# Kernel tuning notes

Measured on AMD Instinct MI355X. Metric: run time of the kernel, lower is better.

## Reference

```python
import jax, jax.numpy as jnp
import numpy as np

N, M, D = 8192, 32768, 256

def setup_inputs() -> dict:
    key = jax.random.key(0)
    k1, k2 = jax.random.split(key)
    image_embs = jax.random.normal(k1, (N, D), dtype=jnp.float32)
    text_embs = jax.random.normal(k2, (M, D), dtype=jnp.float32)
    return {"image_embs": image_embs, "text_embs": text_embs, "k": 10}

def reference(image_embs, text_embs, k):
    # sims: [N, M] similarity matrix (cosine if inputs are pre-normalized)
    sims = image_embs @ text_embs.T
    _, idx = jax.lax.top_k(sims, k)
    return idx.astype(jnp.int32)
```

## Files before the change

kernel.cpp:

```cpp
#include <hip/hip_runtime.h>
#include <hip/hip_bf16.h>
#include <stdint.h>

#define N_ROWS 8192
#define M_COLS 32768
#define D_DIM  256
#define KSEL   10
#define THRMUL 2.75f
#define SEG    40
#define NSEGS  8
#define CSLOT  5
#define NKEEP  16
#define NPAD   32

typedef __bf16              bf16x8 __attribute__((ext_vector_type(8)));
typedef float               f32x4  __attribute__((ext_vector_type(4)));
typedef unsigned short      u16x8  __attribute__((ext_vector_type(8)));
typedef unsigned long long  u64;

__device__ __forceinline__ unsigned short f2bf_rne(float f) {
  unsigned u = __float_as_uint(f);
  u += 0x7FFFu + ((u >> 16) & 1u);
  return (unsigned short)(u >> 16);
}

__device__ __forceinline__ int lanecount_lt(unsigned long long m) {
  return __builtin_amdgcn_mbcnt_hi((unsigned)(m >> 32),
                                   __builtin_amdgcn_mbcnt_lo((unsigned)m, 0));
}

#if __has_builtin(__builtin_amdgcn_global_load_lds)
typedef const __attribute__((address_space(1))) char* gp_t;
typedef __attribute__((address_space(3)))       char* lp_t;
#endif

__device__ __forceinline__ void stage64k(const char* __restrict__ gsrc,
                                         unsigned short* lds, int wid, int lane) {
#if __has_builtin(__builtin_amdgcn_global_load_lds)
#pragma unroll
  for (int i = 0; i < 16; ++i) {
    int off = (wid * 16 + i) * 1024 + lane * 16;
    __builtin_amdgcn_global_load_lds((gp_t)(gsrc + off), (lp_t)((char*)lds + off),
                                     16, 0, 0);
  }
#else
  const u16x8* __restrict__ s = (const u16x8*)gsrc;
  u16x8* d = (u16x8*)lds;
  int t = wid * 64 + lane;
#pragma unroll
  for (int i = 0; i < 16; ++i) d[t + i * 256] = s[t + i * 256];
#endif
}

__global__ __launch_bounds__(256, 2) void cvt_swz_kernel(
    const float* __restrict__ inA, unsigned short* __restrict__ outA,
    const float* __restrict__ inB, unsigned short* __restrict__ outB,
    float* __restrict__ thr) {
  __shared__ alignas(16) unsigned short sm[4224 * 8];
  const int tid = threadIdx.x;
  const int isA = blockIdx.x < (N_ROWS / 128);
  const int tile = isA ? blockIdx.x : blockIdx.x - (N_ROWS / 128);
  const float4* __restrict__ src =
      (const float4*)((isA ? inA : inB) + (size_t)tile * 128 * D_DIM);
  u16x8* __restrict__ dst =
      (u16x8*)((isA ? outA : outB) + (size_t)tile * 128 * D_DIM);

#pragma unroll
  for (int i = 0; i < 16; ++i) {
    int u = i * 256 + tid;
    float4 a = src[u * 2], b = src[u * 2 + 1];
    u16x8 o;
    o[0] = f2bf_rne(a.x); o[1] = f2bf_rne(a.y); o[2] = f2bf_rne(a.z); o[3] = f2bf_rne(a.w);
    o[4] = f2bf_rne(b.x); o[5] = f2bf_rne(b.y); o[6] = f2bf_rne(b.z); o[7] = f2bf_rne(b.w);
    ((u16x8*)sm)[u + (u >> 5)] = o;
  }
  __syncthreads();
#pragma unroll
  for (int i = 0; i < 16; ++i) {
    int o = i * 256 + tid;
    int g = o >> 9, s = (o >> 6) & 7, q = (o >> 4) & 3, m = o & 15;
    int u = ((g * 16 + m) << 5) + s * 4 + q;
    dst[o] = ((const u16x8*)sm)[u + (u >> 5)];
  }

  if (isA) {
    int row = tid >> 1, half = tid & 1;
    const float4* __restrict__ rp =
        (const float4*)(inA + ((size_t)tile * 128 + row) * D_DIM + half * 128);
    float s = 0.f;
#pragma unroll
    for (int j = 0; j < 32; ++j) {
      float4 a = rp[j];
      s += a.x * a.x + a.y * a.y + a.z * a.z + a.w * a.w;
    }
    s += __shfl_xor(s, 1);
    if (half == 0) thr[tile * 128 + row] = THRMUL * sqrtf(s);
  }
}

__global__ __launch_bounds__(256, 2) void gemm_filter_kernel(
    const unsigned short* __restrict__ Ab, const unsigned short* __restrict__ Bb,
    const float* __restrict__ thr,
    int* __restrict__ cnt_seg, u64* __restrict__ cand) {
  __shared__ alignas(16) unsigned short sm[32 * 1024];
  __shared__ float    thr_s[128];
  __shared__ unsigned lcnt[128];

  const int tid  = threadIdx.x;
  const int lane = tid & 63;
  const int wid  = tid >> 6;
  const int wm   = wid >> 1;
  const int wn   = wid & 1;
  const int quad = lane >> 4;
  const int m16  = lane & 15;

  const int bid    = blockIdx.x;
  const int msplit = bid & 7;
  const int rowb   = bid >> 3;
  const int row0   = rowb * 128;
  const int rot    = (bid * 23) & 63;

  stage64k((const char*)Ab + (size_t)rowb * 65536, sm, wid, lane);
  if (tid < 128) { thr_s[tid] = thr[row0 + tid]; lcnt[tid] = 0u; }
  __syncthreads();

  bf16x8 afrag[4][8];
#pragma unroll
  for (int tm = 0; tm < 4; ++tm)
#pragma unroll
    for (int s = 0; s < 8; ++s)
      afrag[tm][s] = ((const bf16x8*)sm)[(wm * 4 + tm) * 512 + s * 64 + lane];
  float thrv[4][4];
#pragma unroll
  for (int tm = 0; tm < 4; ++tm)
#pragma unroll
    for (int r = 0; r < 4; ++r)
      thrv[tm][r] = thr_s[wm * 64 + tm * 16 + quad * 4 + r];
  __syncthreads();

  const u16x8* __restrict__ Bsplit =
      (const u16x8*)((const char*)Bb + (size_t)msplit * 2097152);
  const f32x4 fzero = {0.f, 0.f, 0.f, 0.f};

  bf16x8 bfrag[8][2];
  {
    const u16x8* __restrict__ Bt = Bsplit + (size_t)rot * 2048;
#pragma unroll
    for (int s = 0; s < 4; ++s)
#pragma unroll
      for (int tn = 0; tn < 2; ++tn)
        bfrag[s][tn] = (bf16x8)Bt[(wn * 2 + tn) * 512 + s * 64 + lane];
  }

  for (int i = 0; i < 64; ++i) {
    const int t   = (rot + i) & 63;
    const int tn2 = (rot + i + 1) & 63;
    const u16x8* __restrict__ Bt = Bsplit + (size_t)t * 2048;
    const u16x8* __restrict__ Bn = Bsplit + (size_t)tn2 * 2048;

    f32x4 acc[4][2];
#pragma unroll
    for (int a_ = 0; a_ < 4; ++a_)
#pragma unroll
      for (int b_ = 0; b_ < 2; ++b_) acc[a_][b_] = fzero;

#pragma unroll
    for (int s = 0; s < 8; ++s) {
      const u16x8* __restrict__ src = (s < 4) ? Bt : Bn;
      const int ss = (s + 4) & 7;
#pragma unroll
      for (int tn = 0; tn < 2; ++tn)
        bfrag[ss][tn] = (bf16x8)src[(wn * 2 + tn) * 512 + ss * 64 + lane];
#pragma unroll
      for (int tm = 0; tm < 4; ++tm)
#pragma unroll
        for (int tn = 0; tn < 2; ++tn)
          acc[tm][tn] = __builtin_amdgcn_mfma_f32_16x16x32_bf16(
              afrag[tm][s], bfrag[s][tn], acc[tm][tn], 0, 0, 0);
    }

#pragma unroll
    for (int tm = 0; tm < 4; ++tm) {
#pragma unroll
      for (int tn = 0; tn < 2; ++tn) {
#pragma unroll
        for (int r = 0; r < 4; ++r) {
          float v = acc[tm][tn][r];
          if (v > thrv[tm][r]) {
            int lrow = wm * 64 + tm * 16 + quad * 4 + r;
            unsigned slot = atomicAdd(&lcnt[lrow], 1u);
            if (slot < SEG) {
              int gcol = msplit * 4096 + t * 64 + wn * 32 + tn * 16 + m16;
              u64 pk = ((u64)__float_as_uint(v) << 32) | (unsigned)gcol;
              cand[((size_t)(row0 + lrow) * NSEGS + msplit) * SEG + slot] = pk;
            }
          }
        }
      }
    }
  }
  __syncthreads();

  if (tid < 128) {
    unsigned c = lcnt[tid];
    cnt_seg[(size_t)(row0 + tid) * NSEGS + msplit] = (int)(c < SEG ? c : SEG);
  }
}

__global__ __launch_bounds__(256) void select_rescore_kernel(
    const float* __restrict__ A, const float* __restrict__ B,
    const int* __restrict__ cnt_seg, const u64* __restrict__ cand,
    int* __restrict__ out) {
  __shared__ int    sel_s[4][NPAD];
  __shared__ double ex_s[4][NPAD];

  const int wid  = threadIdx.x >> 6;
  const int lane = threadIdx.x & 63;
  const int r    = blockIdx.x * 4 + wid;

  unsigned key[CSLOT];
  int      id[CSLOT];
#pragma unroll
  for (int j = 0; j < CSLOT; ++j) {
    int p   = lane + j * 64;
    int seg = p / SEG;
    int off = p - seg * SEG;
    int c   = cnt_seg[(size_t)r * NSEGS + seg];
    if (off < c) {
      u64 pk = cand[((size_t)r * NSEGS + seg) * SEG + off];
      key[j] = (unsigned)(pk >> 32);
      id[j]  = (int)(unsigned)(pk & 0xffffffffu);
    } else {
      key[j] = 0u;
      id[j]  = 0x7fffffff;
    }
  }

  unsigned cur = 0;
  for (int b = 30; b >= 8; --b) {
    unsigned candk = cur | (1u << b);
    int c = 0;
#pragma unroll
    for (int j = 0; j < CSLOT; ++j)
      c += __popcll(__ballot(key[j] >= candk));
    if (c >= NKEEP) cur = candk;
  }

  int base = 0;
#pragma unroll
  for (int j = 0; j < CSLOT; ++j) {
    unsigned long long m = __ballot(key[j] >= cur && key[j] != 0u);
    int pos = base + lanecount_lt(m);
    if (key[j] >= cur && key[j] != 0u && pos < NPAD) sel_s[wid][pos] = id[j];
    base += __popcll(m);
  }
  int kcount = base < NPAD ? base : NPAD;
  for (int p = kcount + lane; p < NPAD; p += 64) sel_s[wid][p] = -1;
  __syncthreads();

  const int cand4 = lane >> 2;
  const int half  = lane & 3;
  const float4* __restrict__ A4 = (const float4*)A;
  const float4* __restrict__ B4 = (const float4*)B;
#pragma unroll
  for (int pass = 0; pass < 2; ++pass) {
    int slot = pass * 16 + cand4;
    int idx  = sel_s[wid][slot];
    if (idx >= 0) {
      double acc0 = 0.0, acc1 = 0.0;
#pragma unroll
      for (int j = 0; j < 16; ++j) {
        float4 a4 = A4[(size_t)r * 64 + half * 16 + j];
        float4 b4 = B4[(size_t)idx * 64 + half * 16 + j];
        acc0 += (double)a4.x * b4.x + (double)a4.y * b4.y;
        acc1 += (double)a4.z * b4.z + (double)a4.w * b4.w;
      }
      double tot = acc0 + acc1;
      tot += __shfl_xor(tot, 1);
      tot += __shfl_xor(tot, 2);
      if (half == 0) ex_s[wid][slot] = tot;
    } else if (half == 0) {
      ex_s[wid][slot] = -1.0e300;
    }
  }
  __syncthreads();

  double myex = (lane < NPAD) ? ex_s[wid][lane] : -1.0e300;
  int    myid = (lane < NPAD) ? sel_s[wid][lane] : 0x7fffffff;
  if (myid < 0) { myex = -1.0e300; myid = 0x7fffffff; }
#pragma unroll
  for (int p = 0; p < KSEL; ++p) {
    double be = myex; int bi = myid;
    for (int off = 32; off > 0; off >>= 1) {
      double oe = __shfl_xor(be, off);
      int    oi = __shfl_xor(bi, off);
      if (oe > be || (oe == be && oi < bi)) { be = oe; bi = oi; }
    }
    if (lane == 0) out[(size_t)r * KSEL + p] = bi;
    if (myid == bi) { myex = -1.0e300; myid = 0x7fffffff; }
  }
}

extern "C" void kernel_launch(void* const* d_in, const int* in_sizes, int n_in,
                              void* d_out, int out_size, void* d_ws, size_t ws_size,
                              hipStream_t stream) {
  (void)in_sizes; (void)n_in; (void)out_size; (void)ws_size;
  const float* img = (const float*)d_in[0];
  const float* txt = (const float*)d_in[1];
  int* out = (int*)d_out;

  char* ws = (char*)d_ws;
  unsigned short* Ab = (unsigned short*)ws;
  unsigned short* Bb = (unsigned short*)(ws + ((size_t)4 << 20));
  float* thr     = (float*)(ws + ((size_t)20 << 20));
  int*   cnt_seg = (int*)  (ws + ((size_t)20 << 20) + (64 << 10));
  u64*   cand    = (u64*)  (ws + ((size_t)21 << 20));

  cvt_swz_kernel<<<(N_ROWS + M_COLS) / 128, 256, 0, stream>>>(img, Ab, txt, Bb, thr);

  gemm_filter_kernel<<<512, 256, 0, stream>>>(Ab, Bb, thr, cnt_seg, cand);

  select_rescore_kernel<<<N_ROWS / 4, 256, 0, stream>>>(img, txt, cnt_seg, cand, out);
}
```

Before: 291.7 us.

## Switch filter GEMM from bf16 to fp8 e4m3 and widen the rescore candidate set

Inputs are now quantized to fp8 e4m3 instead of bf16, and the filter GEMM uses fp8 MFMA instructions with A fragments loaded straight from global memory rather than staged through LDS. This halves the bytes moved for the converted matrices and doubles MFMA throughput per instruction. To make up for the larger quantization error, the kept candidates per row go from 16 to 32, and the exact fp64 rescore handles 64 padded slots over four passes. The risks are extra rescore work, and candidates being missed if the fp8 error is larger than the threshold margin or the widened selection allows.

```diff
diff --git a/kernel.cpp b/kernel.cpp
--- a/kernel.cpp
+++ b/kernel.cpp
@@ -10,18 +10,33 @@
 #define SEG    40
 #define NSEGS  8
 #define CSLOT  5
-#define NKEEP  16
-#define NPAD   32
-
-typedef __bf16              bf16x8 __attribute__((ext_vector_type(8)));
+#define NKEEP  32
+#define NPAD   64
+
 typedef float               f32x4  __attribute__((ext_vector_type(4)));
-typedef unsigned short      u16x8  __attribute__((ext_vector_type(8)));
 typedef unsigned long long  u64;
 
-__device__ __forceinline__ unsigned short f2bf_rne(float f) {
+__device__ __forceinline__ unsigned char f2e4m3(float f) {
   unsigned u = __float_as_uint(f);
-  u += 0x7FFFu + ((u >> 16) & 1u);
-  return (unsigned short)(u >> 16);
+  unsigned sgn = (u >> 24) & 0x80u;
+  int E = (int)((u >> 23) & 0xffu) - 127;
+  unsigned m = u & 0x7fffffu;
+  if (E >= -6) {
+    unsigned keep = m >> 20;
+    unsigned rest = m & 0xfffffu;
+    keep += (rest > 0x80000u || (rest == 0x80000u && (keep & 1u))) ? 1u : 0u;
+    unsigned val = ((unsigned)(E + 7) << 3) + keep;
+    if (val > 0x7eu) val = 0x7eu;
+    return (unsigned char)(sgn | val);
+  }
+  if (E < -10) return (unsigned char)sgn;
+  unsigned mant = m | 0x800000u;
+  int shift = 23 - (E + 9);
+  unsigned keep = mant >> shift;
+  unsigned rem  = mant & ((1u << shift) - 1u);
+  unsigned half = 1u << (shift - 1);
+  keep += (rem > half || (rem == half && (keep & 1u))) ? 1u : 0u;
+  return (unsigned char)(sgn | keep);
 }
 
 __device__ __forceinline__ int lanecount_lt(unsigned long long m) {
@@ -29,58 +44,40 @@
                                    __builtin_amdgcn_mbcnt_lo((unsigned)m, 0));
 }
 
-#if __has_builtin(__builtin_amdgcn_global_load_lds)
-typedef const __attribute__((address_space(1))) char* gp_t;
-typedef __attribute__((address_space(3)))       char* lp_t;
-#endif
-
-__device__ __forceinline__ void stage64k(const char* __restrict__ gsrc,
-                                         unsigned short* lds, int wid, int lane) {
-#if __has_builtin(__builtin_amdgcn_global_load_lds)
-#pragma unroll
-  for (int i = 0; i < 16; ++i) {
-    int off = (wid * 16 + i) * 1024 + lane * 16;
-    __builtin_amdgcn_global_load_lds((gp_t)(gsrc + off), (lp_t)((char*)lds + off),
-                                     16, 0, 0);
-  }
-#else
-  const u16x8* __restrict__ s = (const u16x8*)gsrc;
-  u16x8* d = (u16x8*)lds;
-  int t = wid * 64 + lane;
-#pragma unroll
-  for (int i = 0; i < 16; ++i) d[t + i * 256] = s[t + i * 256];
-#endif
-}
-
 __global__ __launch_bounds__(256, 2) void cvt_swz_kernel(
-    const float* __restrict__ inA, unsigned short* __restrict__ outA,
-    const float* __restrict__ inB, unsigned short* __restrict__ outB,
+    const float* __restrict__ inA, unsigned char* __restrict__ outA,
+    const float* __restrict__ inB, unsigned char* __restrict__ outB,
     float* __restrict__ thr) {
-  __shared__ alignas(16) unsigned short sm[4224 * 8];
+  __shared__ alignas(16) char sm[128 * 264];
   const int tid = threadIdx.x;
   const int isA = blockIdx.x < (N_ROWS / 128);
   const int tile = isA ? blockIdx.x : blockIdx.x - (N_ROWS / 128);
   const float4* __restrict__ src =
       (const float4*)((isA ? inA : inB) + (size_t)tile * 128 * D_DIM);
-  u16x8* __restrict__ dst =
-      (u16x8*)((isA ? outA : outB) + (size_t)tile * 128 * D_DIM);
-
-#pragma unroll
-  for (int i = 0; i < 16; ++i) {
+  unsigned char* __restrict__ dst = (isA ? outA : outB) + (size_t)tile * 32768;
+
+#pragma unroll
+  for (int i = 0; i < 32; ++i) {
     int u = i * 256 + tid;
-    float4 a = src[u * 2], b = src[u * 2 + 1];
-    u16x8 o;
-    o[0] = f2bf_rne(a.x); o[1] = f2bf_rne(a.y); o[2] = f2bf_rne(a.z); o[3] = f2bf_rne(a.w);
-    o[4] = f2bf_rne(b.x); o[5] = f2bf_rne(b.y); o[6] = f2bf_rne(b.z); o[7] = f2bf_rne(b.w);
-    ((u16x8*)sm)[u + (u >> 5)] = o;
-  }
-  __syncthreads();
-#pragma unroll
-  for (int i = 0; i < 16; ++i) {
-    int o = i * 256 + tid;
-    int g = o >> 9, s = (o >> 6) & 7, q = (o >> 4) & 3, m = o & 15;
-    int u = ((g * 16 + m) << 5) + s * 4 + q;
-    dst[o] = ((const u16x8*)sm)[u + (u >> 5)];
+    float4 a = src[u];
+    int e = u * 4;
+    int row = e >> 8, k = e & 255;
+    unsigned pk = (unsigned)f2e4m3(a.x) | ((unsigned)f2e4m3(a.y) << 8) |
+                  ((unsigned)f2e4m3(a.z) << 16) | ((unsigned)f2e4m3(a.w) << 24);
+    *(unsigned*)(sm + row * 264 + k) = pk;
+  }
+  __syncthreads();
+#pragma unroll
+  for (int i = 0; i < 8; ++i) {
+    int g = i * 256 + tid;
+    int pn = g >> 10, o = g & 1023;
+    int ln = o & 63, s = (o >> 6) & 7, p = o >> 9;
+    int item = pn * 64 + p * 32 + (ln & 15);
+    int k = s * 32 + (ln >> 4) * 8;
+    u64 lo = *(const u64*)(sm + item * 264 + k);
+    u64 hi = *(const u64*)(sm + (item + 16) * 264 + k);
+    ulong2 v; v.x = lo; v.y = hi;
+    *(ulong2*)(dst + (size_t)g * 16) = v;
   }
 
   if (isA) {
@@ -99,10 +96,9 @@
 }
 
 __global__ __launch_bounds__(256, 2) void gemm_filter_kernel(
-    const unsigned short* __restrict__ Ab, const unsigned short* __restrict__ Bb,
+    const ulong2* __restrict__ Ab, const ulong2* __restrict__ Bb,
     const float* __restrict__ thr,
     int* __restrict__ cnt_seg, u64* __restrict__ cand) {
-  __shared__ alignas(16) unsigned short sm[32 * 1024];
   __shared__ float    thr_s[128];
   __shared__ unsigned lcnt[128];
 
@@ -120,43 +116,43 @@
   const int row0   = rowb * 128;
   const int rot    = (bid * 23) & 63;
 
-  stage64k((const char*)Ab + (size_t)rowb * 65536, sm, wid, lane);
   if (tid < 128) { thr_s[tid] = thr[row0 + tid]; lcnt[tid] = 0u; }
-  __syncthreads();
-
-  bf16x8 afrag[4][8];
-#pragma unroll
-  for (int tm = 0; tm < 4; ++tm)
-#pragma unroll
-    for (int s = 0; s < 8; ++s)
-      afrag[tm][s] = ((const bf16x8*)sm)[(wm * 4 + tm) * 512 + s * 64 + lane];
+
+  const ulong2* __restrict__ Ap = Ab + (size_t)(rowb * 2 + wm) * 1024;
+  long long afrag[4][8];
+#pragma unroll
+  for (int h = 0; h < 2; ++h)
+#pragma unroll
+    for (int s = 0; s < 8; ++s) {
+      ulong2 v = Ap[(h * 8 + s) * 64 + lane];
+      afrag[h * 2 + 0][s] = (long long)v.x;
+      afrag[h * 2 + 1][s] = (long long)v.y;
+    }
+
+  __syncthreads();
   float thrv[4][4];
 #pragma unroll
   for (int tm = 0; tm < 4; ++tm)
 #pragma unroll
     for (int r = 0; r < 4; ++r)
       thrv[tm][r] = thr_s[wm * 64 + tm * 16 + quad * 4 + r];
-  __syncthreads();
-
-  const u16x8* __restrict__ Bsplit =
-      (const u16x8*)((const char*)Bb + (size_t)msplit * 2097152);
+
+  const ulong2* __restrict__ Bsplit = Bb + (size_t)msplit * 65536;
   const f32x4 fzero = {0.f, 0.f, 0.f, 0.f};
 
-  bf16x8 bfrag[8][2];
+  ulong2 bfrag[8];
   {
-    const u16x8* __restrict__ Bt = Bsplit + (size_t)rot * 2048;
+    const ulong2* __restrict__ Bt = Bsplit + (size_t)rot * 1024;
 #pragma unroll
     for (int s = 0; s < 4; ++s)
-#pragma unroll
-      for (int tn = 0; tn < 2; ++tn)
-        bfrag[s][tn] = (bf16x8)Bt[(wn * 2 + tn) * 512 + s * 64 + lane];
+      bfrag[s] = Bt[(wn * 8 + s) * 64 + lane];
   }
 
   for (int i = 0; i < 64; ++i) {
     const int t   = (rot + i) & 63;
     const int tn2 = (rot + i + 1) & 63;
-    const u16x8* __restrict__ Bt = Bsplit + (size_t)t * 2048;
-    const u16x8* __restrict__ Bn = Bsplit + (size_t)tn2 * 2048;
+    const ulong2* __restrict__ Bt = Bsplit + (size_t)t * 1024;
+    const ulong2* __restrict__ Bn = Bsplit + (size_t)tn2 * 1024;
 
     f32x4 acc[4][2];
 #pragma unroll
@@ -166,17 +162,16 @@
 
 #pragma unroll
     for (int s = 0; s < 8; ++s) {
-      const u16x8* __restrict__ src = (s < 4) ? Bt : Bn;
+      const ulong2* __restrict__ src = (s < 4) ? Bt : Bn;
       const int ss = (s + 4) & 7;
-#pragma unroll
-      for (int tn = 0; tn < 2; ++tn)
-        bfrag[ss][tn] = (bf16x8)src[(wn * 2 + tn) * 512 + ss * 64 + lane];
-#pragma unroll
-      for (int tm = 0; tm < 4; ++tm)
-#pragma unroll
-        for (int tn = 0; tn < 2; ++tn)
-          acc[tm][tn] = __builtin_amdgcn_mfma_f32_16x16x32_bf16(
-              afrag[tm][s], bfrag[s][tn], acc[tm][tn], 0, 0, 0);
+      bfrag[ss] = src[(wn * 8 + ss) * 64 + lane];
+#pragma unroll
+      for (int tm = 0; tm < 4; ++tm) {
+        acc[tm][0] = __builtin_amdgcn_mfma_f32_16x16x32_fp8_fp8(
+            afrag[tm][s], (long long)bfrag[s].x, acc[tm][0], 0, 0, 0);
+        acc[tm][1] = __builtin_amdgcn_mfma_f32_16x16x32_fp8_fp8(
+            afrag[tm][s], (long long)bfrag[s].y, acc[tm][1], 0, 0, 0);
+      }
     }
 
 #pragma unroll
@@ -263,7 +258,7 @@
   const float4* __restrict__ A4 = (const float4*)A;
   const float4* __restrict__ B4 = (const float4*)B;
 #pragma unroll
-  for (int pass = 0; pass < 2; ++pass) {
+  for (int pass = 0; pass < 4; ++pass) {
     int slot = pass * 16 + cand4;
     int idx  = sel_s[wid][slot];
     if (idx >= 0) {
@@ -285,8 +280,8 @@
   }
   __syncthreads();
 
-  double myex = (lane < NPAD) ? ex_s[wid][lane] : -1.0e300;
-  int    myid = (lane < NPAD) ? sel_s[wid][lane] : 0x7fffffff;
+  double myex = ex_s[wid][lane];
+  int    myid = sel_s[wid][lane];
   if (myid < 0) { myex = -1.0e300; myid = 0x7fffffff; }
 #pragma unroll
   for (int p = 0; p < KSEL; ++p) {
@@ -310,15 +305,16 @@
   int* out = (int*)d_out;
 
   char* ws = (char*)d_ws;
-  unsigned short* Ab = (unsigned short*)ws;
-  unsigned short* Bb = (unsigned short*)(ws + ((size_t)4 << 20));
-  float* thr     = (float*)(ws + ((size_t)20 << 20));
-  int*   cnt_seg = (int*)  (ws + ((size_t)20 << 20) + (64 << 10));
-  u64*   cand    = (u64*)  (ws + ((size_t)21 << 20));
+  unsigned char* Ab = (unsigned char*)ws;
+  unsigned char* Bb = (unsigned char*)(ws + ((size_t)2 << 20));
+  float* thr     = (float*)(ws + ((size_t)12 << 20));
+  int*   cnt_seg = (int*)  (ws + ((size_t)12 << 20) + (64 << 10));
+  u64*   cand    = (u64*)  (ws + ((size_t)13 << 20));
 
   cvt_swz_kernel<<<(N_ROWS + M_COLS) / 128, 256, 0, stream>>>(img, Ab, txt, Bb, thr);
 
-  gemm_filter_kernel<<<512, 256, 0, stream>>>(Ab, Bb, thr, cnt_seg, cand);
+  gemm_filter_kernel<<<512, 256, 0, stream>>>((const ulong2*)Ab, (const ulong2*)Bb,
+                                              thr, cnt_seg, cand);
 
   select_rescore_kernel<<<N_ROWS / 4, 256, 0, stream>>>(img, txt, cnt_seg, cand, out);
 }
```

After: 289.4 us. No clear change (-0.8%).
